# Performance work log

Measured on AMD Instinct MI355X. Metric: run time of the kernel, lower is better.

The kernel has to match this reference:

```python
import jax, jax.numpy as jnp
import numpy as np

L, S, B, DIN, D, H, F = 12, 512, 4, 768, 1024, 16, 4096
HD = D // H  # 64


def setup_inputs() -> dict:
    key = jax.random.key(0)
    ks = jax.random.split(key, 16)
    std = 0.02

    def w(k, shape):
        return jax.random.normal(k, shape, jnp.float32) * std

    inp = {
        "segments": jax.random.normal(ks[0], (S, B, DIN), jnp.float32),
        "durations": jax.random.uniform(ks[1], (S, B, 1), jnp.float32),
        "padding_mask": jax.random.randint(ks[2], (B, S), 0, 2) > 0,
        # input projections
        "Wproj": w(ks[3], (DIN, D)), "bproj": jnp.zeros((D,), jnp.float32),
        "Wdur": w(ks[4], (1, D)), "bdur": jnp.zeros((D,), jnp.float32),
        # per-layer stacked params (leading dim L)
        "ln1_g": jnp.ones((L, D), jnp.float32), "ln1_b": jnp.zeros((L, D), jnp.float32),
        "Wq": w(ks[5], (L, D, D)), "bq": jnp.zeros((L, D), jnp.float32),
        "Wk": w(ks[6], (L, D, D)), "bk": jnp.zeros((L, D), jnp.float32),
        "Wv": w(ks[7], (L, D, D)), "bv": jnp.zeros((L, D), jnp.float32),
        "Wo": w(ks[8], (L, D, D)), "bo": jnp.zeros((L, D), jnp.float32),
        "ln2_g": jnp.ones((L, D), jnp.float32), "ln2_b": jnp.zeros((L, D), jnp.float32),
        "Wff1": w(ks[9], (L, D, F)), "bff1": jnp.zeros((L, F), jnp.float32),
        "Wff2": w(ks[10], (L, F, D)), "bff2": jnp.zeros((L, D), jnp.float32),
    }
    return inp


def _rope_cache(seq_len):
    inv_freq = 1.0 / (10000.0 ** (jnp.arange(0, HD, 2, dtype=jnp.float32) / HD))
    t = jnp.arange(seq_len, dtype=jnp.float32)
    freqs = jnp.outer(t, inv_freq)                 # [S, HD/2]
    emb = jnp.concatenate([freqs, freqs], axis=-1)  # [S, HD]
    return jnp.cos(emb), jnp.sin(emb)


def _ln(x, g, b, eps=1e-5):
    m = jnp.mean(x, axis=-1, keepdims=True)
    v = jnp.var(x, axis=-1, keepdims=True)
    return (x - m) / jnp.sqrt(v + eps) * g + b


def _encoder(segments, durations, padding_mask, Wproj, bproj, Wdur, bdur,
             ln1_g, ln1_b, Wq, bq, Wk, bk, Wv, bv, Wo, bo,
             ln2_g, ln2_b, Wff1, bff1, Wff2, bff2):
    cos, sin = _rope_cache(S)  # [S, HD] each, broadcast over [B, H, S, HD]
    key_mask = padding_mask[:, None, None, :]  # [B,1,1,S]
    scale = 1.0 / jnp.sqrt(jnp.float32(HD))

    def rope(x):  # x: [B, H, S, HD]
        x1, x2 = jnp.split(x, 2, axis=-1)
        rotated = jnp.concatenate([-x2, x1], axis=-1)
        return x * cos + rotated * sin

    # x: [S, B, D]
    x = segments @ Wproj + bproj + durations @ Wdur + bdur

    def layer(x, p):
        g1, b1, wq, bq_, wk, bk_, wv, bv_, wo, bo_, g2, b2, w1, bf1, w2, bf2 = p
        h = _ln(x, g1, b1)

        def heads(w, bb):  # [S,B,D] -> [B,H,S,HD]
            return (h @ w + bb).reshape(S, B, H, HD).transpose(1, 2, 0, 3)

        q = rope(heads(wq, bq_))
        k = rope(heads(wk, bk_))
        v = heads(wv, bv_)
        scores = jnp.einsum('bhqd,bhkd->bhqk', q, k) * scale  # [B,H,S,S]
        scores = jnp.where(key_mask, -jnp.inf, scores)
        probs = jax.nn.softmax(scores, axis=-1)
        attn = jnp.einsum('bhqk,bhkd->bhqd', probs, v)  # [B,H,S,HD]
        attn = attn.transpose(2, 0, 1, 3).reshape(S, B, D)
        x = x + attn @ wo + bo_
        h2 = _ln(x, g2, b2)
        x = x + jax.nn.gelu(h2 @ w1 + bf1, approximate=False) @ w2 + bf2
        return x, None

    xs = (ln1_g, ln1_b, Wq, bq, Wk, bk, Wv, bv, Wo, bo,
          ln2_g, ln2_b, Wff1, bff1, Wff2, bff2)
    x, _ = jax.lax.scan(layer, x, xs)
    return x


def reference(segments, durations, padding_mask, Wproj, bproj, Wdur, bdur,
              ln1_g, ln1_b, Wq, bq, Wk, bk, Wv, bv, Wo, bo,
              ln2_g, ln2_b, Wff1, bff1, Wff2, bff2):
    return _encoder(segments, durations, padding_mask, Wproj, bproj, Wdur, bdur,
                    ln1_g, ln1_b, Wq, bq, Wk, bk, Wv, bv, Wo, bo,
                    ln2_g, ln2_b, Wff1, bff1, Wff2, bff2)
```

## Files before the change

### kernel.cpp

```cpp
#include <hip/hip_runtime.h>
#include <math.h>

typedef __bf16 bf16;
typedef float f32x4 __attribute__((ext_vector_type(4)));
typedef __bf16 bf16x8 __attribute__((ext_vector_type(8)));
typedef __bf16 bf16x4 __attribute__((ext_vector_type(4)));

__device__ __forceinline__ void gld16(const bf16* g, bf16* l)
{
    __builtin_amdgcn_global_load_lds(
        (const __attribute__((address_space(1))) void*)g,
        (__attribute__((address_space(3))) void*)l, 16, 0, 0);
}

__device__ __forceinline__ float gelu_exact(float x)
{
    return 0.5f * x * (1.0f + erff(x * 0.70710678118654752f));
}

template <int EPI>
__launch_bounds__(256, 2)
__global__ void gemm_bt(const bf16* __restrict__ A, const bf16* __restrict__ Bt,
                        const float* __restrict__ bias, int K, int N,
                        float* __restrict__ fout, bf16* __restrict__ bout,
                        const float* __restrict__ res, const float* __restrict__ bias2,
                        const float* __restrict__ dvec, const float* __restrict__ wdur)
{
    __shared__ alignas(16) bf16 As[128 * 32];
    __shared__ alignas(16) bf16 Bs[128 * 32];
    const int tid = threadIdx.x;
    const int lane = tid & 63, wave = tid >> 6;
    const int quad = lane >> 4, l16 = lane & 15;
    const int wr = wave >> 1, wc = wave & 1;
    const int mBase = blockIdx.y * 128, nBase = blockIdx.x * 128;

    f32x4 zero = {0.f, 0.f, 0.f, 0.f};
    f32x4 acc[4][4];
#pragma unroll
    for (int i = 0; i < 4; ++i)
#pragma unroll
        for (int j = 0; j < 4; ++j) acc[i][j] = zero;

    const int c0 = wave * 128 + lane;
    const int c1 = c0 + 64;
    const bf16* Ag0 = A + (size_t)(mBase + (c0 >> 2)) * K + (c0 & 3) * 8;
    const bf16* Ag1 = A + (size_t)(mBase + (c1 >> 2)) * K + (c1 & 3) * 8;
    const bf16* Bg0 = Bt + (size_t)(nBase + (c0 >> 2)) * K + (c0 & 3) * 8;
    const bf16* Bg1 = Bt + (size_t)(nBase + (c1 >> 2)) * K + (c1 & 3) * 8;
    bf16* Al0 = As + (size_t)(wave * 128) * 8;
    bf16* Al1 = As + (size_t)(wave * 128 + 64) * 8;
    bf16* Bl0 = Bs + (size_t)(wave * 128) * 8;
    bf16* Bl1 = Bs + (size_t)(wave * 128 + 64) * 8;

    for (int k0 = 0; k0 < K; k0 += 32) {
        gld16(Ag0 + k0, Al0);
        gld16(Ag1 + k0, Al1);
        gld16(Bg0 + k0, Bl0);
        gld16(Bg1 + k0, Bl1);
        __syncthreads();
        bf16x8 af[4], bfr[4];
#pragma unroll
        for (int t = 0; t < 4; ++t) {
            af[t]  = *(const bf16x8*)(As + (wr * 64 + t * 16 + l16) * 32 + quad * 8);
            bfr[t] = *(const bf16x8*)(Bs + (wc * 64 + t * 16 + l16) * 32 + quad * 8);
        }
#pragma unroll
        for (int i = 0; i < 4; ++i)
#pragma unroll
            for (int j = 0; j < 4; ++j)
                acc[i][j] = __builtin_amdgcn_mfma_f32_16x16x32_bf16(af[i], bfr[j], acc[i][j], 0, 0, 0);
        __syncthreads();
    }

#pragma unroll
    for (int i = 0; i < 4; ++i) {
        const int row0 = mBase + wr * 64 + i * 16 + quad * 4;
#pragma unroll
        for (int j = 0; j < 4; ++j) {
            const int col = nBase + wc * 64 + j * 16 + l16;
            const float bs = bias[col];
#pragma unroll
            for (int r = 0; r < 4; ++r) {
                const int row = row0 + r;
                float v = acc[i][j][r] + bs;
                if (EPI == 0) {
                    bout[(size_t)row * N + col] = (bf16)v;
                } else if (EPI == 1) {
                    bout[(size_t)row * N + col] = (bf16)gelu_exact(v);
                } else if (EPI == 2) {
                    fout[(size_t)row * N + col] = res[(size_t)row * N + col] + v;
                } else {
                    v += bias2[col] + dvec[row] * wdur[col];
                    fout[(size_t)row * N + col] = v;
                }
            }
        }
    }
}

__launch_bounds__(256)
__global__ void ln_kernel(const float* __restrict__ x, const float* __restrict__ g,
                          const float* __restrict__ b, bf16* __restrict__ out)
{
    const int row = blockIdx.x, tid = threadIdx.x;
    const int lane = tid & 63, wave = tid >> 6;
    float4 v = ((const float4*)(x + (size_t)row * 1024))[tid];
    float s = v.x + v.y + v.z + v.w;
    float q = v.x * v.x + v.y * v.y + v.z * v.z + v.w * v.w;
#pragma unroll
    for (int o = 32; o > 0; o >>= 1) {
        s += __shfl_down(s, o, 64);
        q += __shfl_down(q, o, 64);
    }
    __shared__ float red[8];
    if (lane == 0) { red[wave] = s; red[4 + wave] = q; }
    __syncthreads();
    s = red[0] + red[1] + red[2] + red[3];
    q = red[4] + red[5] + red[6] + red[7];
    const float mean = s * 0.0009765625f;
    const float var = q * 0.0009765625f - mean * mean;
    const float rstd = rsqrtf(var + 1e-5f);
    float4 gv = ((const float4*)g)[tid];
    float4 bv = ((const float4*)b)[tid];
    bf16x4 o4;
    o4[0] = (bf16)((v.x - mean) * rstd * gv.x + bv.x);
    o4[1] = (bf16)((v.y - mean) * rstd * gv.y + bv.y);
    o4[2] = (bf16)((v.z - mean) * rstd * gv.z + bv.z);
    o4[3] = (bf16)((v.w - mean) * rstd * gv.w + bv.w);
    ((bf16x4*)(out + (size_t)row * 1024))[tid] = o4;
}

__launch_bounds__(256)
__global__ void rope_kernel(bf16* __restrict__ qkv)
{
    const int id = blockIdx.x * 256 + threadIdx.x;
    const int i = id & 31;
    const int head = (id >> 5) & 15;
    const int qk = (id >> 9) & 1;
    const int m = id >> 10;
    const int s = m >> 2;
    const size_t base = (size_t)m * 3072 + (size_t)qk * 1024 + head * 64 + i;
    const float x1 = (float)qkv[base];
    const float x2 = (float)qkv[base + 32];
    const float inv = expf((float)i * -0.28782313662425574f);
    const float ang = (float)s * inv;
    const float c = cosf(ang), sn = sinf(ang);
    qkv[base]      = (bf16)(x1 * c - x2 * sn);
    qkv[base + 32] = (bf16)(x2 * c + x1 * sn);
}

__launch_bounds__(256)
__global__ void vt_kernel(const bf16* __restrict__ qkv, bf16* __restrict__ vT)
{
    __shared__ bf16 tile[32][33];
    const int tid = threadIdx.x;
    const int tx = tid & 31, ty = tid >> 5;
    const int bh = blockIdx.z, b = bh >> 4, h = bh & 15;
    const int s0 = blockIdx.x * 32, d0 = blockIdx.y * 32;
#pragma unroll
    for (int i = 0; i < 4; ++i) {
        const int s = s0 + ty + i * 8;
        tile[ty + i * 8][tx] = qkv[(size_t)(s * 4 + b) * 3072 + 2048 + h * 64 + d0 + tx];
    }
    __syncthreads();
#pragma unroll
    for (int i = 0; i < 4; ++i) {
        const int d = d0 + ty + i * 8;
        vT[((size_t)(b * 16 + h) * 64 + d) * 512 + s0 + tx] = tile[tx][ty + i * 8];
    }
}

__launch_bounds__(256, 2)
__global__ void attn_kernel(const bf16* __restrict__ qkv, const bf16* __restrict__ vT,
                            const int* __restrict__ mask, bf16* __restrict__ out)
{
    __shared__ alignas(16) bf16 Ks[64 * 72];
    __shared__ alignas(16) bf16 Vts[64 * 72];
    __shared__ alignas(16) bf16 Pscr[4][32 * 72];
    __shared__ float mbias[512];

    const int tid = threadIdx.x;
    const int lane = tid & 63, wave = tid >> 6;
    const int quad = lane >> 4, l16 = lane & 15;
    const int qt = blockIdx.x, h = blockIdx.y, b = blockIdx.z;

    for (int i = tid; i < 512; i += 256)
        mbias[i] = mask[b * 512 + i] ? -1e30f : 0.0f;

    bf16x8 qf[2][2];
#pragma unroll
    for (int t = 0; t < 2; ++t)
#pragma unroll
        for (int c = 0; c < 2; ++c) {
            const int s = qt * 128 + wave * 32 + t * 16 + l16;
            qf[t][c] = *(const bf16x8*)(qkv + (size_t)(s * 4 + b) * 3072 + h * 64 + c * 32 + quad * 8);
        }

    f32x4 zero = {0.f, 0.f, 0.f, 0.f};
    f32x4 O[2][4];
    float m_run[2][4], l_run[2][4];
#pragma unroll
    for (int t = 0; t < 2; ++t) {
#pragma unroll
        for (int d = 0; d < 4; ++d) O[t][d] = zero;
#pragma unroll
        for (int r = 0; r < 4; ++r) { m_run[t][r] = -10000.f; l_run[t][r] = 0.f; }
    }

    for (int kt = 0; kt < 8; ++kt) {
        bf16x8 kreg[2], vreg[2];
#pragma unroll
        for (int i = 0; i < 2; ++i) {
            const int c = wave * 128 + i * 64 + lane;
            const int kr = c >> 3, dc = c & 7;
            kreg[i] = *(const bf16x8*)(qkv + (size_t)((kt * 64 + kr) * 4 + b) * 3072 + 1024 + h * 64 + dc * 8);
            vreg[i] = *(const bf16x8*)(vT + ((size_t)(b * 16 + h) * 64 + kr) * 512 + kt * 64 + dc * 8);
        }
        __syncthreads();
#pragma unroll
        for (int i = 0; i < 2; ++i) {
            const int c = wave * 128 + i * 64 + lane;
            const int kr = c >> 3, dc = c & 7;
            *(bf16x8*)(Ks + kr * 72 + dc * 8)  = kreg[i];
            *(bf16x8*)(Vts + kr * 72 + dc * 8) = vreg[i];
        }
        __syncthreads();

        bf16x8 bk_[4][2];
#pragma unroll
        for (int tc = 0; tc < 4; ++tc)
#pragma unroll
            for (int c = 0; c < 2; ++c)
                bk_[tc][c] = *(const bf16x8*)(Ks + (tc * 16 + l16) * 72 + c * 32 + quad * 8);

        f32x4 sf[2][4];
#pragma unroll
        for (int t = 0; t < 2; ++t)
#pragma unroll
            for (int tc = 0; tc < 4; ++tc) {
                f32x4 z = zero;
                z = __builtin_amdgcn_mfma_f32_16x16x32_bf16(qf[t][0], bk_[tc][0], z, 0, 0, 0);
                z = __builtin_amdgcn_mfma_f32_16x16x32_bf16(qf[t][1], bk_[tc][1], z, 0, 0, 0);
                sf[t][tc] = z;
            }

#pragma unroll
        for (int t = 0; t < 2; ++t) {
#pragma unroll
            for (int tc = 0; tc < 4; ++tc) {
                const float mb = mbias[kt * 64 + tc * 16 + l16];
#pragma unroll
                for (int r = 0; r < 4; ++r)
                    sf[t][tc][r] = sf[t][tc][r] * 0.125f + mb;
            }
#pragma unroll
            for (int r = 0; r < 4; ++r) {
                float tm = fmaxf(fmaxf(sf[t][0][r], sf[t][1][r]), fmaxf(sf[t][2][r], sf[t][3][r]));
                tm = fmaxf(tm, __shfl_xor(tm, 1, 64));
                tm = fmaxf(tm, __shfl_xor(tm, 2, 64));
                tm = fmaxf(tm, __shfl_xor(tm, 4, 64));
                tm = fmaxf(tm, __shfl_xor(tm, 8, 64));
                const float mn = fmaxf(m_run[t][r], tm);
                const float alpha = __expf(m_run[t][r] - mn);
                m_run[t][r] = mn;
                float rs = 0.f;
#pragma unroll
                for (int tc = 0; tc < 4; ++tc) {
                    const float p = __expf(sf[t][tc][r] - mn);
                    sf[t][tc][r] = p;
                    rs += p;
                }
                rs += __shfl_xor(rs, 1, 64);
                rs += __shfl_xor(rs, 2, 64);
                rs += __shfl_xor(rs, 4, 64);
                rs += __shfl_xor(rs, 8, 64);
                l_run[t][r] = l_run[t][r] * alpha + rs;
#pragma unroll
                for (int d = 0; d < 4; ++d) O[t][d][r] *= alpha;
            }
#pragma unroll
            for (int tc = 0; tc < 4; ++tc)
#pragma unroll
                for (int r = 0; r < 4; ++r)
                    Pscr[wave][(t * 16 + quad * 4 + r) * 72 + tc * 16 + l16] = (bf16)sf[t][tc][r];
        }

        bf16x8 bv_[4][2];
#pragma unroll
        for (int d = 0; d < 4; ++d)
#pragma unroll
            for (int c = 0; c < 2; ++c)
                bv_[d][c] = *(const bf16x8*)(Vts + (d * 16 + l16) * 72 + c * 32 + quad * 8);
#pragma unroll
        for (int t = 0; t < 2; ++t) {
            bf16x8 pa0 = *(const bf16x8*)(&Pscr[wave][(t * 16 + l16) * 72 + quad * 8]);
            bf16x8 pa1 = *(const bf16x8*)(&Pscr[wave][(t * 16 + l16) * 72 + 32 + quad * 8]);
#pragma unroll
            for (int d = 0; d < 4; ++d) {
                O[t][d] = __builtin_amdgcn_mfma_f32_16x16x32_bf16(pa0, bv_[d][0], O[t][d], 0, 0, 0);
                O[t][d] = __builtin_amdgcn_mfma_f32_16x16x32_bf16(pa1, bv_[d][1], O[t][d], 0, 0, 0);
            }
        }
        __syncthreads();
    }

#pragma unroll
    for (int t = 0; t < 2; ++t)
#pragma unroll
        for (int d = 0; d < 4; ++d) {
            const int col = h * 64 + d * 16 + l16;
#pragma unroll
            for (int r = 0; r < 4; ++r) {
                const int s = qt * 128 + wave * 32 + t * 16 + quad * 4 + r;
                out[(size_t)(s * 4 + b) * 1024 + col] = (bf16)(O[t][d][r] / l_run[t][r]);
            }
        }
}

__device__ __forceinline__ void trans_tile32(const float* __restrict__ src, bf16* __restrict__ dst,
                                             int R, int C, int r0, int c0, int tid)
{
    __shared__ float tile[32][33];
    const int tx = tid & 31, ty = tid >> 5;
#pragma unroll
    for (int i = 0; i < 4; ++i)
        tile[ty + i * 8][tx] = src[(size_t)(r0 + ty + i * 8) * C + c0 + tx];
    __syncthreads();
#pragma unroll
    for (int i = 0; i < 4; ++i)
        dst[(size_t)(c0 + ty + i * 8) * R + r0 + tx] = (bf16)tile[tx][ty + i * 8];
}

__launch_bounds__(256)
__global__ void wtrans(const float* __restrict__ src, bf16* __restrict__ dst, int R, int C)
{
    trans_tile32(src, dst, R, C, blockIdx.y * 32, blockIdx.x * 32, threadIdx.x);
}

__launch_bounds__(256)
__global__ void wtrans_layer(const float* __restrict__ Wq, const float* __restrict__ Wk,
                             const float* __restrict__ Wv, const float* __restrict__ Wo,
                             const float* __restrict__ Wf1, const float* __restrict__ Wf2,
                             int l, bf16* __restrict__ qkvT, bf16* __restrict__ oT,
                             bf16* __restrict__ f1T, bf16* __restrict__ f2T)
{
    const int id = blockIdx.x;
    const float* src;
    bf16* dst;
    int R, C, r0, c0;
    if (id < 3072) {
        const int f = id >> 10, t = id & 1023;
        src = (f == 0 ? Wq : (f == 1 ? Wk : Wv)) + (size_t)l * 1048576;
        dst = qkvT + (size_t)f * 1048576;
        R = 1024; C = 1024; r0 = (t >> 5) * 32; c0 = (t & 31) * 32;
    } else if (id < 4096) {
        const int t = id - 3072;
        src = Wo + (size_t)l * 1048576; dst = oT;
        R = 1024; C = 1024; r0 = (t >> 5) * 32; c0 = (t & 31) * 32;
    } else if (id < 8192) {
        const int t = id - 4096;
        src = Wf1 + (size_t)l * 4194304; dst = f1T;
        R = 1024; C = 4096; r0 = (t >> 7) * 32; c0 = (t & 127) * 32;
    } else {
        const int t = id - 8192;
        src = Wf2 + (size_t)l * 4194304; dst = f2T;
        R = 4096; C = 1024; r0 = (t >> 5) * 32; c0 = (t & 31) * 32;
    }
    trans_tile32(src, dst, R, C, r0, c0, threadIdx.x);
}

__launch_bounds__(256)
__global__ void packb_kernel(const float* __restrict__ bq, const float* __restrict__ bk,
                             const float* __restrict__ bv, float* __restrict__ bqkv)
{
    const int id = blockIdx.x * 256 + threadIdx.x;
    if (id >= 12 * 3072) return;
    const int l = id / 3072, j = id - l * 3072;
    float v;
    if (j < 1024) v = bq[l * 1024 + j];
    else if (j < 2048) v = bk[l * 1024 + j - 1024];
    else v = bv[l * 1024 + j - 2048];
    bqkv[id] = v;
}

__launch_bounds__(256)
__global__ void cvt_kernel(const float* __restrict__ in, bf16* __restrict__ out)
{
    const int id = blockIdx.x * 256 + threadIdx.x;
    float4 v = ((const float4*)in)[id];
    bf16x4 o;
    o[0] = (bf16)v.x; o[1] = (bf16)v.y; o[2] = (bf16)v.z; o[3] = (bf16)v.w;
    ((bf16x4*)out)[id] = o;
}

extern "C" void kernel_launch(void* const* d_in, const int* in_sizes, int n_in,
                              void* d_out, int out_size, void* d_ws, size_t ws_size,
                              hipStream_t stream)
{
    const float* segments  = (const float*)d_in[0];
    const float* durations = (const float*)d_in[1];
    const int*   pmask     = (const int*)d_in[2];
    const float* Wproj = (const float*)d_in[3];
    const float* bproj = (const float*)d_in[4];
    const float* Wdur  = (const float*)d_in[5];
    const float* bdur  = (const float*)d_in[6];
    const float* ln1_g = (const float*)d_in[7];
    const float* ln1_b = (const float*)d_in[8];
    const float* Wq = (const float*)d_in[9];
    const float* bq = (const float*)d_in[10];
    const float* Wk = (const float*)d_in[11];
    const float* bk = (const float*)d_in[12];
    const float* Wv = (const float*)d_in[13];
    const float* bv = (const float*)d_in[14];
    const float* Wo = (const float*)d_in[15];
    const float* bo = (const float*)d_in[16];
    const float* ln2_g = (const float*)d_in[17];
    const float* ln2_b = (const float*)d_in[18];
    const float* Wff1 = (const float*)d_in[19];
    const float* bff1 = (const float*)d_in[20];
    const float* Wff2 = (const float*)d_in[21];
    const float* bff2 = (const float*)d_in[22];

    char* ws = (char*)d_ws;
    size_t off = 0;
    auto alloc = [&](size_t n) { char* p = ws + off; off += (n + 255) & ~(size_t)255; return p; };
    bf16* qkvT  = (bf16*)alloc((size_t)3072 * 1024 * 2);
    bf16* oT    = (bf16*)alloc((size_t)1024 * 1024 * 2);
    bf16* f1T   = (bf16*)alloc((size_t)4096 * 1024 * 2);
    bf16* f2T   = (bf16*)alloc((size_t)1024 * 4096 * 2);
    bf16* projT = (bf16*)alloc((size_t)1024 * 768 * 2);
    float* bqkv = (float*)alloc((size_t)12 * 3072 * 4);
    bf16* segsB = (bf16*)alloc((size_t)2048 * 768 * 2);
    float* x    = (float*)alloc((size_t)2048 * 1024 * 4);
    bf16* hbuf  = (bf16*)alloc((size_t)2048 * 1024 * 2);
    bf16* qkv   = (bf16*)alloc((size_t)2048 * 3072 * 2);
    bf16* vTb   = (bf16*)alloc((size_t)64 * 64 * 512 * 2);
    bf16* attnO = (bf16*)alloc((size_t)2048 * 1024 * 2);
    bf16* ffh   = (bf16*)alloc((size_t)2048 * 4096 * 2);
    float* xout = (float*)d_out;

    dim3 blk(256);
    wtrans<<<dim3(32, 24, 1), blk, 0, stream>>>(Wproj, projT, 768, 1024);
    packb_kernel<<<dim3(144), blk, 0, stream>>>(bq, bk, bv, bqkv);
    cvt_kernel<<<dim3(1536), blk, 0, stream>>>(segments, segsB);
    gemm_bt<3><<<dim3(8, 16), blk, 0, stream>>>(segsB, projT, bproj, 768, 1024,
                                                x, nullptr, nullptr, bdur, durations, Wdur);
    for (int l = 0; l < 12; ++l) {
        wtrans_layer<<<dim3(12288), blk, 0, stream>>>(Wq, Wk, Wv, Wo, Wff1, Wff2, l,
                                                      qkvT, oT, f1T, f2T);
        ln_kernel<<<dim3(2048), blk, 0, stream>>>(x, ln1_g + l * 1024, ln1_b + l * 1024, hbuf);
        gemm_bt<0><<<dim3(24, 16), blk, 0, stream>>>(hbuf, qkvT, bqkv + l * 3072, 1024, 3072,
                                                     nullptr, qkv, nullptr, nullptr, nullptr, nullptr);
        rope_kernel<<<dim3(8192), blk, 0, stream>>>(qkv);
        vt_kernel<<<dim3(16, 2, 64), blk, 0, stream>>>(qkv, vTb);
        attn_kernel<<<dim3(4, 16, 4), blk, 0, stream>>>(qkv, vTb, pmask, attnO);
        gemm_bt<2><<<dim3(8, 16), blk, 0, stream>>>(attnO, oT, bo + l * 1024, 1024, 1024,
                                                    x, nullptr, x, nullptr, nullptr, nullptr);
        ln_kernel<<<dim3(2048), blk, 0, stream>>>(x, ln2_g + l * 1024, ln2_b + l * 1024, hbuf);
        gemm_bt<1><<<dim3(32, 16), blk, 0, stream>>>(hbuf, f1T, bff1 + l * 4096, 1024, 4096,
                                                     nullptr, ffh, nullptr, nullptr, nullptr, nullptr);
        float* xo = (l == 11) ? xout : x;
        gemm_bt<2><<<dim3(8, 16), blk, 0, stream>>>(ffh, f2T, bff2 + l * 1024, 4096, 1024,
                                                    xo, nullptr, x, nullptr, nullptr, nullptr);
    }
}
```

Measured before the change: 3.155 ms.

## Fuse RoPE into QKV GEMM, narrow N-tiles, hoist weight transposes

Several changes at once. RoPE is applied in the QKV GEMM epilogue using a precomputed cos/sin table, which removes the separate rope kernel and its extra pass over qkv. The N=1024 GEMMs switch to 64-wide N tiles, doubling the block count from 128 to 256 so more CUs are busy. The per-layer weight transposes are also merged into one launch before the loop that writes all 12 layers into larger workspace buffers. This uses 12x more workspace and puts the whole transpose cost up front.

```diff
diff --git a/kernel.cpp b/kernel.cpp
--- a/kernel.cpp
+++ b/kernel.cpp
@@ -18,63 +18,98 @@
     return 0.5f * x * (1.0f + erff(x * 0.70710678118654752f));
 }
 
-template <int EPI>
+template <int EPI, int BN>
 __launch_bounds__(256, 2)
 __global__ void gemm_bt(const bf16* __restrict__ A, const bf16* __restrict__ Bt,
                         const float* __restrict__ bias, int K, int N,
                         float* __restrict__ fout, bf16* __restrict__ bout,
                         const float* __restrict__ res, const float* __restrict__ bias2,
-                        const float* __restrict__ dvec, const float* __restrict__ wdur)
-{
+                        const float* __restrict__ dvec, const float* __restrict__ wdur,
+                        const float2* __restrict__ rtab)
+{
+    constexpr int MI = (BN == 128) ? 4 : 2;
     __shared__ alignas(16) bf16 As[128 * 32];
-    __shared__ alignas(16) bf16 Bs[128 * 32];
+    __shared__ alignas(16) bf16 Bs[BN * 32];
     const int tid = threadIdx.x;
     const int lane = tid & 63, wave = tid >> 6;
     const int quad = lane >> 4, l16 = lane & 15;
-    const int wr = wave >> 1, wc = wave & 1;
-    const int mBase = blockIdx.y * 128, nBase = blockIdx.x * 128;
+    const int wr = (BN == 128) ? (wave >> 1) : wave;
+    const int wc = (BN == 128) ? (wave & 1) : 0;
+    const int rowBase = (BN == 128) ? wr * 64 : wr * 32;
+    const int mBase = blockIdx.y * 128, nBase = blockIdx.x * BN;
 
     f32x4 zero = {0.f, 0.f, 0.f, 0.f};
-    f32x4 acc[4][4];
-#pragma unroll
-    for (int i = 0; i < 4; ++i)
+    f32x4 acc[MI][4];
+#pragma unroll
+    for (int i = 0; i < MI; ++i)
 #pragma unroll
         for (int j = 0; j < 4; ++j) acc[i][j] = zero;
 
-    const int c0 = wave * 128 + lane;
-    const int c1 = c0 + 64;
-    const bf16* Ag0 = A + (size_t)(mBase + (c0 >> 2)) * K + (c0 & 3) * 8;
-    const bf16* Ag1 = A + (size_t)(mBase + (c1 >> 2)) * K + (c1 & 3) * 8;
-    const bf16* Bg0 = Bt + (size_t)(nBase + (c0 >> 2)) * K + (c0 & 3) * 8;
-    const bf16* Bg1 = Bt + (size_t)(nBase + (c1 >> 2)) * K + (c1 & 3) * 8;
+    const int ca0 = wave * 128 + lane;
+    const int ca1 = ca0 + 64;
+    const bf16* Ag0 = A + (size_t)(mBase + (ca0 >> 2)) * K + (ca0 & 3) * 8;
+    const bf16* Ag1 = A + (size_t)(mBase + (ca1 >> 2)) * K + (ca1 & 3) * 8;
     bf16* Al0 = As + (size_t)(wave * 128) * 8;
     bf16* Al1 = As + (size_t)(wave * 128 + 64) * 8;
-    bf16* Bl0 = Bs + (size_t)(wave * 128) * 8;
+    const int cb0 = (BN == 128) ? ca0 : (wave * 64 + lane);
+    const bf16* Bg0 = Bt + (size_t)(nBase + (cb0 >> 2)) * K + (cb0 & 3) * 8;
+    const bf16* Bg1 = Bt + (size_t)(nBase + (ca1 >> 2)) * K + (ca1 & 3) * 8;
+    bf16* Bl0 = (BN == 128) ? (Bs + (size_t)(wave * 128) * 8) : (Bs + (size_t)(wave * 64) * 8);
     bf16* Bl1 = Bs + (size_t)(wave * 128 + 64) * 8;
 
     for (int k0 = 0; k0 < K; k0 += 32) {
         gld16(Ag0 + k0, Al0);
         gld16(Ag1 + k0, Al1);
         gld16(Bg0 + k0, Bl0);
-        gld16(Bg1 + k0, Bl1);
+        if (BN == 128) gld16(Bg1 + k0, Bl1);
         __syncthreads();
-        bf16x8 af[4], bfr[4];
-#pragma unroll
-        for (int t = 0; t < 4; ++t) {
-            af[t]  = *(const bf16x8*)(As + (wr * 64 + t * 16 + l16) * 32 + quad * 8);
+        bf16x8 af[MI], bfr[4];
+#pragma unroll
+        for (int t = 0; t < MI; ++t)
+            af[t] = *(const bf16x8*)(As + (rowBase + t * 16 + l16) * 32 + quad * 8);
+#pragma unroll
+        for (int t = 0; t < 4; ++t)
             bfr[t] = *(const bf16x8*)(Bs + (wc * 64 + t * 16 + l16) * 32 + quad * 8);
-        }
-#pragma unroll
-        for (int i = 0; i < 4; ++i)
+#pragma unroll
+        for (int i = 0; i < MI; ++i)
 #pragma unroll
             for (int j = 0; j < 4; ++j)
                 acc[i][j] = __builtin_amdgcn_mfma_f32_16x16x32_bf16(af[i], bfr[j], acc[i][j], 0, 0, 0);
         __syncthreads();
     }
 
-#pragma unroll
-    for (int i = 0; i < 4; ++i) {
-        const int row0 = mBase + wr * 64 + i * 16 + quad * 4;
+    if (EPI == 4) {
+        const bool isqk = (nBase + wc * 64) < 2048;
+#pragma unroll
+        for (int i = 0; i < MI; ++i) {
+            const int row0 = mBase + rowBase + i * 16 + quad * 4;
+#pragma unroll
+            for (int j = 0; j < 2; ++j) {
+                const int col = nBase + wc * 64 + j * 16 + l16;
+                const float b1 = bias[col], b2 = bias[col + 32];
+#pragma unroll
+                for (int r = 0; r < 4; ++r) {
+                    const int row = row0 + r;
+                    float v1 = acc[i][j][r] + b1;
+                    float v2 = acc[i][j + 2][r] + b2;
+                    if (isqk) {
+                        const int s = row >> 2;
+                        const float2 cs = rtab[s * 32 + j * 16 + l16];
+                        const float o1 = v1 * cs.x - v2 * cs.y;
+                        const float o2 = v2 * cs.x + v1 * cs.y;
+                        v1 = o1; v2 = o2;
+                    }
+                    bout[(size_t)row * N + col]      = (bf16)v1;
+                    bout[(size_t)row * N + col + 32] = (bf16)v2;
+                }
+            }
+        }
+        return;
+    }
+
+#pragma unroll
+    for (int i = 0; i < MI; ++i) {
+        const int row0 = mBase + rowBase + i * 16 + quad * 4;
 #pragma unroll
         for (int j = 0; j < 4; ++j) {
             const int col = nBase + wc * 64 + j * 16 + l16;
@@ -131,22 +166,13 @@
 }
 
 __launch_bounds__(256)
-__global__ void rope_kernel(bf16* __restrict__ qkv)
+__global__ void rtab_kernel(float2* __restrict__ tab)
 {
     const int id = blockIdx.x * 256 + threadIdx.x;
-    const int i = id & 31;
-    const int head = (id >> 5) & 15;
-    const int qk = (id >> 9) & 1;
-    const int m = id >> 10;
-    const int s = m >> 2;
-    const size_t base = (size_t)m * 3072 + (size_t)qk * 1024 + head * 64 + i;
-    const float x1 = (float)qkv[base];
-    const float x2 = (float)qkv[base + 32];
+    const int s = id >> 5, i = id & 31;
     const float inv = expf((float)i * -0.28782313662425574f);
-    const float ang = (float)s * inv;
-    const float c = cosf(ang), sn = sinf(ang);
-    qkv[base]      = (bf16)(x1 * c - x2 * sn);
-    qkv[base + 32] = (bf16)(x2 * c + x1 * sn);
+    const float a = (float)s * inv;
+    tab[id] = make_float2(cosf(a), sinf(a));
 }
 
 __launch_bounds__(256)
@@ -338,32 +364,33 @@
 }
 
 __launch_bounds__(256)
-__global__ void wtrans_layer(const float* __restrict__ Wq, const float* __restrict__ Wk,
-                             const float* __restrict__ Wv, const float* __restrict__ Wo,
-                             const float* __restrict__ Wf1, const float* __restrict__ Wf2,
-                             int l, bf16* __restrict__ qkvT, bf16* __restrict__ oT,
-                             bf16* __restrict__ f1T, bf16* __restrict__ f2T)
+__global__ void wtrans_all(const float* __restrict__ Wq, const float* __restrict__ Wk,
+                           const float* __restrict__ Wv, const float* __restrict__ Wo,
+                           const float* __restrict__ Wf1, const float* __restrict__ Wf2,
+                           bf16* __restrict__ qkvT, bf16* __restrict__ oT,
+                           bf16* __restrict__ f1T, bf16* __restrict__ f2T)
 {
     const int id = blockIdx.x;
+    const int l = blockIdx.y;
     const float* src;
     bf16* dst;
     int R, C, r0, c0;
     if (id < 3072) {
         const int f = id >> 10, t = id & 1023;
         src = (f == 0 ? Wq : (f == 1 ? Wk : Wv)) + (size_t)l * 1048576;
-        dst = qkvT + (size_t)f * 1048576;
+        dst = qkvT + (size_t)l * 3145728 + (size_t)f * 1048576;
         R = 1024; C = 1024; r0 = (t >> 5) * 32; c0 = (t & 31) * 32;
     } else if (id < 4096) {
         const int t = id - 3072;
-        src = Wo + (size_t)l * 1048576; dst = oT;
+        src = Wo + (size_t)l * 1048576; dst = oT + (size_t)l * 1048576;
         R = 1024; C = 1024; r0 = (t >> 5) * 32; c0 = (t & 31) * 32;
     } else if (id < 8192) {
         const int t = id - 4096;
-        src = Wf1 + (size_t)l * 4194304; dst = f1T;
+        src = Wf1 + (size_t)l * 4194304; dst = f1T + (size_t)l * 4194304;
         R = 1024; C = 4096; r0 = (t >> 7) * 32; c0 = (t & 127) * 32;
     } else {
         const int t = id - 8192;
-        src = Wf2 + (size_t)l * 4194304; dst = f2T;
+        src = Wf2 + (size_t)l * 4194304; dst = f2T + (size_t)l * 4194304;
         R = 4096; C = 1024; r0 = (t >> 5) * 32; c0 = (t & 31) * 32;
     }
     trans_tile32(src, dst, R, C, r0, c0, threadIdx.x);
@@ -424,12 +451,13 @@
     char* ws = (char*)d_ws;
     size_t off = 0;
     auto alloc = [&](size_t n) { char* p = ws + off; off += (n + 255) & ~(size_t)255; return p; };
-    bf16* qkvT  = (bf16*)alloc((size_t)3072 * 1024 * 2);
-    bf16* oT    = (bf16*)alloc((size_t)1024 * 1024 * 2);
-    bf16* f1T   = (bf16*)alloc((size_t)4096 * 1024 * 2);
-    bf16* f2T   = (bf16*)alloc((size_t)1024 * 4096 * 2);
+    bf16* qkvT  = (bf16*)alloc((size_t)12 * 3072 * 1024 * 2);
+    bf16* oT    = (bf16*)alloc((size_t)12 * 1024 * 1024 * 2);
+    bf16* f1T   = (bf16*)alloc((size_t)12 * 4096 * 1024 * 2);
+    bf16* f2T   = (bf16*)alloc((size_t)12 * 1024 * 4096 * 2);
     bf16* projT = (bf16*)alloc((size_t)1024 * 768 * 2);
     float* bqkv = (float*)alloc((size_t)12 * 3072 * 4);
+    float2* rtab = (float2*)alloc((size_t)512 * 32 * 8);
     bf16* segsB = (bf16*)alloc((size_t)2048 * 768 * 2);
     float* x    = (float*)alloc((size_t)2048 * 1024 * 4);
     bf16* hbuf  = (bf16*)alloc((size_t)2048 * 1024 * 2);
@@ -441,26 +469,30 @@
 
     dim3 blk(256);
     wtrans<<<dim3(32, 24, 1), blk, 0, stream>>>(Wproj, projT, 768, 1024);
+    wtrans_all<<<dim3(12288, 12), blk, 0, stream>>>(Wq, Wk, Wv, Wo, Wff1, Wff2,
+                                                    qkvT, oT, f1T, f2T);
     packb_kernel<<<dim3(144), blk, 0, stream>>>(bq, bk, bv, bqkv);
+    rtab_kernel<<<dim3(64), blk, 0, stream>>>(rtab);
     cvt_kernel<<<dim3(1536), blk, 0, stream>>>(segments, segsB);
-    gemm_bt<3><<<dim3(8, 16), blk, 0, stream>>>(segsB, projT, bproj, 768, 1024,
-                                                x, nullptr, nullptr, bdur, durations, Wdur);
+    gemm_bt<3, 64><<<dim3(16, 16), blk, 0, stream>>>(segsB, projT, bproj, 768, 1024,
+                                                     x, nullptr, nullptr, bdur, durations, Wdur, nullptr);
     for (int l = 0; l < 12; ++l) {
-        wtrans_layer<<<dim3(12288), blk, 0, stream>>>(Wq, Wk, Wv, Wo, Wff1, Wff2, l,
-                                                      qkvT, oT, f1T, f2T);
         ln_kernel<<<dim3(2048), blk, 0, stream>>>(x, ln1_g + l * 1024, ln1_b + l * 1024, hbuf);
-        gemm_bt<0><<<dim3(24, 16), blk, 0, stream>>>(hbuf, qkvT, bqkv + l * 3072, 1024, 3072,
-                                                     nullptr, qkv, nullptr, nullptr, nullptr, nullptr);
-        rope_kernel<<<dim3(8192), blk, 0, stream>>>(qkv);
+        gemm_bt<4, 128><<<dim3(24, 16), blk, 0, stream>>>(hbuf, qkvT + (size_t)l * 3145728,
+                                                          bqkv + l * 3072, 1024, 3072,
+                                                          nullptr, qkv, nullptr, nullptr, nullptr, nullptr, rtab);
         vt_kernel<<<dim3(16, 2, 64), blk, 0, stream>>>(qkv, vTb);
         attn_kernel<<<dim3(4, 16, 4), blk, 0, stream>>>(qkv, vTb, pmask, attnO);
-        gemm_bt<2><<<dim3(8, 16), blk, 0, stream>>>(attnO, oT, bo + l * 1024, 1024, 1024,
-                                                    x, nullptr, x, nullptr, nullptr, nullptr);
+        gemm_bt<2, 64><<<dim3(16, 16), blk, 0, stream>>>(attnO, oT + (size_t)l * 1048576,
+                                                         bo + l * 1024, 1024, 1024,
+                                                         x, nullptr, x, nullptr, nullptr, nullptr, nullptr);
         ln_kernel<<<dim3(2048), blk, 0, stream>>>(x, ln2_g + l * 1024, ln2_b + l * 1024, hbuf);
-        gemm_bt<1><<<dim3(32, 16), blk, 0, stream>>>(hbuf, f1T, bff1 + l * 4096, 1024, 4096,
-                                                     nullptr, ffh, nullptr, nullptr, nullptr, nullptr);
+        gemm_bt<1, 128><<<dim3(32, 16), blk, 0, stream>>>(hbuf, f1T + (size_t)l * 4194304,
+                                                          bff1 + l * 4096, 1024, 4096,
+                                                          nullptr, ffh, nullptr, nullptr, nullptr, nullptr, nullptr);
         float* xo = (l == 11) ? xout : x;
-        gemm_bt<2><<<dim3(8, 16), blk, 0, stream>>>(ffh, f2T, bff2 + l * 1024, 4096, 1024,
-                                                    xo, nullptr, x, nullptr, nullptr, nullptr);
-    }
-}
+        gemm_bt<2, 64><<<dim3(16, 16), blk, 0, stream>>>(ffh, f2T + (size_t)l * 4194304,
+                                                         bff2 + l * 1024, 4096, 1024,
+                                                         xo, nullptr, x, nullptr, nullptr, nullptr, nullptr);
+    }
+}
```

Result: slower. 3.347 ms (+6.1%).
